# Optimization experiments

Measured on AMD Instinct MI355X. Metric: run time of the kernel, lower is better.

Reference implementation:

```python
import jax, jax.numpy as jnp
import numpy as np

KERNEL_SIZE = 32
STRIDE = 16


def _block_compress(x, w, pe):
    # x: [B, N, H, D]; w: [K]; pe: [K, D]
    B, N, H, D = x.shape
    M = (N - KERNEL_SIZE) // STRIDE + 1
    # window gather indices: [M, K]
    idx = jnp.arange(M)[:, None] * STRIDE + jnp.arange(KERNEL_SIZE)[None, :]
    xw = x[:, idx]  # [B, M, K, H, D]
    # y = sum_k w[k] * (x_window + pe) / kernel_size
    return jnp.einsum('bmkhd,k->bmhd', xw + pe[None, None, :, None, :], w) / KERNEL_SIZE


def setup_inputs() -> dict:
    key = jax.random.key(0)
    k1, k2, k3, k4, k5, k6, k7 = jax.random.split(key, 7)
    B, N, QH, KH, D, VD = 1, 8192, 32, 2, 128, 128
    return {
        'q': jax.random.normal(k1, (B, N, QH, D), dtype=jnp.float32),
        'k': jax.random.normal(k2, (B, N, KH, D), dtype=jnp.float32),
        'v': jax.random.normal(k3, (B, N, KH, VD), dtype=jnp.float32),
        'w_key': jax.random.normal(k4, (KERNEL_SIZE,), dtype=jnp.float32),
        'pe_key': jax.random.normal(k5, (KERNEL_SIZE, D), dtype=jnp.float32),
        'w_val': jax.random.normal(k6, (KERNEL_SIZE,), dtype=jnp.float32),
        'pe_val': jax.random.normal(k7, (KERNEL_SIZE, VD), dtype=jnp.float32),
    }


def reference(q, k, v, w_key, pe_key, w_val, pe_val):
    ck = _block_compress(k, w_key, pe_key)  # [B, M, KH, D]
    cv = _block_compress(v, w_val, pe_val)  # [B, M, KH, VD]
    B, N, QH, D = q.shape
    M, KH = ck.shape[1], ck.shape[2]
    G = QH // KH  # GQA group size; off_kh = off_qh // G -> qh index = kh*G + g
    sm_scale = D ** -0.5
    qg = q.reshape(B, N, KH, G, D)
    # scores: [B, KH, G, N, M]
    scores = jnp.einsum('bnhgd,bmhd->bhgnm', qg, ck) * sm_scale
    # block-causal mask: query n attends block m iff n >= m*stride + kernel_size - 1
    n_idx = jnp.arange(N)
    m_last = jnp.arange(M) * STRIDE + KERNEL_SIZE - 1
    mask = n_idx[:, None] >= m_last[None, :]  # [N, M]
    scores = jnp.where(mask[None, None, None], scores, -jnp.inf)
    lse = jax.nn.logsumexp(scores, axis=-1)  # [B, KH, G, N]
    # queries before kernel_size-1 have no valid blocks: kernel zeros o and lse
    valid = n_idx >= KERNEL_SIZE - 1
    lse = jnp.where(valid[None, None, None], lse, 0.0)
    p = jnp.exp(scores - lse[..., None])  # exp(-inf - 0) = 0 on invalid rows
    o = jnp.einsum('bhgnm,bmhd->bnhgd', p, cv).reshape(B, N, QH, -1)
    lse = lse.reshape(B, QH, N)
    return o, lse, ck
```

## Files before the change

kernel.cpp:

```cpp
#include <hip/hip_runtime.h>

#define DI __device__ __forceinline__

using f32x4  = __attribute__((ext_vector_type(4))) float;
using bf16x8 = __attribute__((ext_vector_type(8))) short;
using u32x4  = __attribute__((ext_vector_type(4))) unsigned int;

DI unsigned short f2bf(float f) {
    unsigned int u = __float_as_uint(f);
    unsigned int r = u + 0x7FFFu + ((u >> 16) & 1u);
    return (unsigned short)(r >> 16);
}

DI void gload_lds16(const void* g, void* l) {
    __builtin_amdgcn_global_load_lds(
        (const __attribute__((address_space(1))) void*)(unsigned long long)g,
        (__attribute__((address_space(3))) void*)(unsigned int)(unsigned long long)l,
        16, 0, 0);
}

constexpr int N_SEQ = 8192;
constexpr int QH    = 32;
constexpr int KH    = 2;
constexpr int D     = 128;
constexpr int M_CMP = 511;
constexpr int MP    = 512;
constexpr int NCH   = 16;
constexpr int CHUNK_ELEMS = 16 * 64 * 8;
constexpr int HSTRIDE = NCH * CHUNK_ELEMS;

__global__ __launch_bounds__(256)
void compress_kernel(const float* __restrict__ kin, const float* __restrict__ vin,
                     const float* __restrict__ w_key, const float* __restrict__ pe_key,
                     const float* __restrict__ w_val, const float* __restrict__ pe_val,
                     float* __restrict__ ck_out,
                     unsigned short* __restrict__ kvb)
{
    const int m  = blockIdx.x;
    const int t  = threadIdx.x;
    const int hh = t >> 7;
    const int d  = t & 127;
    float acck = 0.f, accv = 0.f;
    if (m < M_CMP) {
        #pragma unroll
        for (int k = 0; k < 32; ++k) {
            float xk = kin[((m*16 + k)*KH + hh)*D + d];
            float xv = vin[((m*16 + k)*KH + hh)*D + d];
            acck += (xk + pe_key[k*D + d]) * w_key[k];
            accv += (xv + pe_val[k*D + d]) * w_val[k];
        }
        acck *= (1.f/32.f);
        accv *= (1.f/32.f);
        ck_out[(m*KH + hh)*D + d] = acck;
    }
    const int c = m >> 5, ml = m & 31;
    {
        const int mt = ml >> 4, colx = ml & 15;
        const int kc = d >> 5, hix = (d >> 3) & 3, e = d & 7;
        kvb[(size_t)hh*HSTRIDE + (((c*16 + mt*4 + kc)*64) + hix*16 + colx)*8 + e] = f2bf(acck);
    }
    {
        const int e   = ((ml >> 4) << 2) + (ml & 3);
        const int hix = (ml >> 2) & 3;
        const int dt  = d >> 4, colx = d & 15;
        kvb[(size_t)hh*HSTRIDE + (((c*16 + 8 + dt)*64) + hix*16 + colx)*8 + e] = f2bf(accv);
    }
}

__global__ __launch_bounds__(256)
void attn_kernel(const float* __restrict__ q,
                 const unsigned short* __restrict__ kvb,
                 float* __restrict__ o,
                 float* __restrict__ lse)
{
    __shared__ __align__(16) unsigned short lds[2][16][64][8];

    const int h    = blockIdx.y;
    const int t    = threadIdx.x;
    const int wid  = t >> 6;
    const int lane = t & 63;
    const int col  = lane & 15;
    const int hi   = lane >> 4;
    const int j    = (blockIdx.x << 2) + wid;

    const int n0r = j;
    const int n1r = N_SEQ - 1 - j;
    const int mcnt0 = (n0r >= 31) ? (((n0r - 31) >> 4) + 1) : 0;
    const int mcnt1 = ((n1r - 31) >> 4) + 1;
    const int n1max = N_SEQ - 1 - (blockIdx.x << 2);
    const int nchb  = (((((n1max - 31) >> 4) + 1) + 31) >> 5);

    const float sm_scale = 0.08838834764831845f;
    const float NEG_INF  = -__builtin_inff();

    bf16x8 qf0[4], qf1[4];
    {
        const float* qp0 = q + ((size_t)n0r*QH + (h << 4) + col)*D + (hi << 3);
        const float* qp1 = q + ((size_t)n1r*QH + (h << 4) + col)*D + (hi << 3);
        #pragma unroll
        for (int kc = 0; kc < 4; ++kc) {
            float4 a0 = *(const float4*)(qp0 + kc*32);
            float4 b0 = *(const float4*)(qp0 + kc*32 + 4);
            float4 a1 = *(const float4*)(qp1 + kc*32);
            float4 b1 = *(const float4*)(qp1 + kc*32 + 4);
            bf16x8 f0, f1;
            f0[0]=(short)f2bf(a0.x*sm_scale); f0[1]=(short)f2bf(a0.y*sm_scale);
            f0[2]=(short)f2bf(a0.z*sm_scale); f0[3]=(short)f2bf(a0.w*sm_scale);
            f0[4]=(short)f2bf(b0.x*sm_scale); f0[5]=(short)f2bf(b0.y*sm_scale);
            f0[6]=(short)f2bf(b0.z*sm_scale); f0[7]=(short)f2bf(b0.w*sm_scale);
            f1[0]=(short)f2bf(a1.x*sm_scale); f1[1]=(short)f2bf(a1.y*sm_scale);
            f1[2]=(short)f2bf(a1.z*sm_scale); f1[3]=(short)f2bf(a1.w*sm_scale);
            f1[4]=(short)f2bf(b1.x*sm_scale); f1[5]=(short)f2bf(b1.y*sm_scale);
            f1[6]=(short)f2bf(b1.z*sm_scale); f1[7]=(short)f2bf(b1.w*sm_scale);
            qf0[kc] = f0; qf1[kc] = f1;
        }
    }

    f32x4 oacc0[8], oacc1[8];
    #pragma unroll
    for (int dt = 0; dt < 8; ++dt) {
        oacc0[dt] = (f32x4){0.f,0.f,0.f,0.f};
        oacc1[dt] = (f32x4){0.f,0.f,0.f,0.f};
    }
    float rmax0 = -3e38f, rmax1 = -3e38f, rsum0 = 0.f, rsum1 = 0.f;

    const unsigned short* kvh = kvb + (size_t)h*HSTRIDE;

    auto STAGE = [&](int buf, int c) {
        const unsigned short* gp = kvh + ((size_t)(c*16 + (wid << 2))*64 + lane)*8;
        #pragma unroll
        for (int p = 0; p < 4; ++p)
            gload_lds16(gp + p*512, &lds[buf][(wid << 2) + p][lane][0]);
    };

    auto SMAX = [&](f32x4 sa, f32x4 sb, int lim, float& rm, float& rs,
                    f32x4* oaccr, unsigned int* pw) {
        float sv[8];
        if (lim < 32) {
            const int mb = hi << 2;
            #pragma unroll
            for (int jj = 0; jj < 4; ++jj) {
                sv[jj]     = (mb + jj      < lim) ? sa[jj] : NEG_INF;
                sv[4 + jj] = (mb + jj + 16 < lim) ? sb[jj] : NEG_INF;
            }
        } else {
            #pragma unroll
            for (int jj = 0; jj < 4; ++jj) { sv[jj] = sa[jj]; sv[4 + jj] = sb[jj]; }
        }
        float pm = fmaxf(fmaxf(fmaxf(sv[0],sv[1]), fmaxf(sv[2],sv[3])),
                         fmaxf(fmaxf(sv[4],sv[5]), fmaxf(sv[6],sv[7])));
        if (!__all(pm <= rm + 8.0f)) {
            float tm = pm;
            tm = fmaxf(tm, __shfl_xor(tm, 16));
            tm = fmaxf(tm, __shfl_xor(tm, 32));
            float nm = fmaxf(rm, tm);
            float sc = __expf(rm - nm);
            rs *= sc;
            #pragma unroll
            for (int dt = 0; dt < 8; ++dt) {
                oaccr[dt][0] *= sc; oaccr[dt][1] *= sc;
                oaccr[dt][2] *= sc; oaccr[dt][3] *= sc;
            }
            rm = nm;
        }
        float p[8];
        #pragma unroll
        for (int i = 0; i < 8; ++i) p[i] = __expf(sv[i] - rm);
        rs += ((p[0]+p[1]) + (p[2]+p[3])) + ((p[4]+p[5]) + (p[6]+p[7]));
        asm("v_cvt_pk_bf16_f32 %0, %1, %2" : "=v"(pw[0]) : "v"(p[0]), "v"(p[1]));
        asm("v_cvt_pk_bf16_f32 %0, %1, %2" : "=v"(pw[1]) : "v"(p[2]), "v"(p[3]));
        asm("v_cvt_pk_bf16_f32 %0, %1, %2" : "=v"(pw[2]) : "v"(p[4]), "v"(p[5]));
        asm("v_cvt_pk_bf16_f32 %0, %1, %2" : "=v"(pw[3]) : "v"(p[6]), "v"(p[7]));
    };

    STAGE(0, 0);
    __syncthreads();

    for (int c = 0; c < nchb; ++c) {
        if (c + 1 < nchb) STAGE((c + 1) & 1, c + 1);

        const int m0 = c << 5;
        const bool a1 = (m0 < mcnt1);
        const bool a0 = (m0 < mcnt0);
        const unsigned short (*L)[64][8] = lds[c & 1];

        f32x4 s10 = (f32x4){0,0,0,0}, s11 = (f32x4){0,0,0,0};
        f32x4 s00 = (f32x4){0,0,0,0}, s01 = (f32x4){0,0,0,0};
        #pragma unroll
        for (int kc = 0; kc < 4; ++kc) {
            bf16x8 ca = *(const bf16x8*)&L[kc][lane][0];
            bf16x8 cb = *(const bf16x8*)&L[4 + kc][lane][0];
            s10 = __builtin_amdgcn_mfma_f32_16x16x32_bf16(ca, qf1[kc], s10, 0, 0, 0);
            s11 = __builtin_amdgcn_mfma_f32_16x16x32_bf16(cb, qf1[kc], s11, 0, 0, 0);
            if (a0) {
                s00 = __builtin_amdgcn_mfma_f32_16x16x32_bf16(ca, qf0[kc], s00, 0, 0, 0);
                s01 = __builtin_amdgcn_mfma_f32_16x16x32_bf16(cb, qf0[kc], s01, 0, 0, 0);
            }
        }
        unsigned int pw1[4], pw0[4];
        if (a1) SMAX(s10, s11, mcnt1 - m0, rmax1, rsum1, oacc1, pw1);
        if (a0) SMAX(s00, s01, mcnt0 - m0, rmax0, rsum0, oacc0, pw0);

        {
            u32x4 b1v = {pw1[0], pw1[1], pw1[2], pw1[3]};
            u32x4 b0v = {pw0[0], pw0[1], pw0[2], pw0[3]};
            #pragma unroll
            for (int dt = 0; dt < 8; ++dt) {
                bf16x8 cv = *(const bf16x8*)&L[8 + dt][lane][0];
                if (a1)
                    asm("v_mfma_f32_16x16x32_bf16 %0, %1, %2, %0"
                        : "+v"(oacc1[dt]) : "v"(cv), "v"(b1v));
                if (a0)
                    asm("v_mfma_f32_16x16x32_bf16 %0, %1, %2, %0"
                        : "+v"(oacc0[dt]) : "v"(cv), "v"(b0v));
            }
        }

        __syncthreads();
    }

    auto EPI = [&](int n, float rm, float rs, f32x4* oaccr, bool valid) {
        float r = rs;
        r += __shfl_xor(r, 16);
        r += __shfl_xor(r, 32);
        const float inv = valid ? (1.0f / r) : 0.0f;
        float* op = o + ((size_t)n*QH + (h << 4) + col)*D + (hi << 2);
        #pragma unroll
        for (int dt = 0; dt < 8; ++dt) {
            f32x4 w = oaccr[dt];
            w[0] *= inv; w[1] *= inv; w[2] *= inv; w[3] *= inv;
            *(f32x4*)(op + dt*16) = w;
        }
        if (lane < 16) {
            float lv = valid ? (rm + __logf(r)) : 0.0f;
            lse[((size_t)(h << 4) + col)*N_SEQ + n] = lv;
        }
    };
    EPI(n0r, rmax0, rsum0, oacc0, mcnt0 > 0);
    EPI(n1r, rmax1, rsum1, oacc1, true);
}

extern "C" void kernel_launch(void* const* d_in, const int* in_sizes, int n_in,
                              void* d_out, int out_size, void* d_ws, size_t ws_size,
                              hipStream_t stream)
{
    const float* q      = (const float*)d_in[0];
    const float* k      = (const float*)d_in[1];
    const float* v      = (const float*)d_in[2];
    const float* w_key  = (const float*)d_in[3];
    const float* pe_key = (const float*)d_in[4];
    const float* w_val  = (const float*)d_in[5];
    const float* pe_val = (const float*)d_in[6];

    float* o   = (float*)d_out;
    float* lse = o + (size_t)N_SEQ * QH * D;
    float* ck  = lse + (size_t)QH * N_SEQ;

    unsigned short* kvb = (unsigned short*)d_ws;

    compress_kernel<<<dim3(MP), dim3(256), 0, stream>>>(
        k, v, w_key, pe_key, w_val, pe_val, ck, kvb);

    attn_kernel<<<dim3(N_SEQ/8, KH), dim3(256), 0, stream>>>(
        q, kvb, o, lse);
}
```

Baseline: 100.5 us.

## Split KV chunks across two wave groups and merge softmax states via LDS

The block grows to 512 threads with two 4-wave groups. Each group processes alternating KV chunks, so the per-query KV loop is split in two. The groups then merge partial max, sum and output accumulators through shared memory before the epilogue. This aims to shorten the serial chunk loop and raise the number of waves in flight, at the cost of larger LDS use (68KB), lower block occupancy and an extra merge phase with barriers.

```diff
diff --git a/kernel.cpp b/kernel.cpp
--- a/kernel.cpp
+++ b/kernel.cpp
@@ -67,21 +67,23 @@
     }
 }
 
-__global__ __launch_bounds__(256)
+__global__ __launch_bounds__(512)
 void attn_kernel(const float* __restrict__ q,
                  const unsigned short* __restrict__ kvb,
                  float* __restrict__ o,
                  float* __restrict__ lse)
 {
-    __shared__ __align__(16) unsigned short lds[2][16][64][8];
+    __shared__ __align__(16) unsigned char smem[69632];
 
     const int h    = blockIdx.y;
     const int t    = threadIdx.x;
     const int wid  = t >> 6;
+    const int grp  = wid >> 2;
+    const int lw   = wid & 3;
     const int lane = t & 63;
     const int col  = lane & 15;
     const int hi   = lane >> 4;
-    const int j    = (blockIdx.x << 2) + wid;
+    const int j    = (blockIdx.x << 2) + lw;
 
     const int n0r = j;
     const int n1r = N_SEQ - 1 - j;
@@ -89,9 +91,14 @@
     const int mcnt1 = ((n1r - 31) >> 4) + 1;
     const int n1max = N_SEQ - 1 - (blockIdx.x << 2);
     const int nchb  = (((((n1max - 31) >> 4) + 1) + 31) >> 5);
+    const int T     = (nchb + 1) >> 1;
 
     const float sm_scale = 0.08838834764831845f;
     const float NEG_INF  = -__builtin_inff();
+
+    auto SB = [&](int idx) {
+        return (unsigned short (*)[64][8])(smem + idx * 16384);
+    };
 
     bf16x8 qf0[4], qf1[4];
     {
@@ -126,11 +133,12 @@
 
     const unsigned short* kvh = kvb + (size_t)h*HSTRIDE;
 
-    auto STAGE = [&](int buf, int c) {
-        const unsigned short* gp = kvh + ((size_t)(c*16 + (wid << 2))*64 + lane)*8;
+    auto STAGE = [&](int bufidx, int c) {
+        const unsigned short* gp = kvh + ((size_t)(c*16 + (lw << 2))*64 + lane)*8;
+        unsigned short (*L)[64][8] = SB(bufidx);
         #pragma unroll
         for (int p = 0; p < 4; ++p)
-            gload_lds16(gp + p*512, &lds[buf][(wid << 2) + p][lane][0]);
+            gload_lds16(gp + p*512, &L[(lw << 2) + p][lane][0]);
     };
 
     auto SMAX = [&](f32x4 sa, f32x4 sb, int lim, float& rm, float& rs,
@@ -173,35 +181,42 @@
         asm("v_cvt_pk_bf16_f32 %0, %1, %2" : "=v"(pw[3]) : "v"(p[6]), "v"(p[7]));
     };
 
-    STAGE(0, 0);
-    __syncthreads();
-
-    for (int c = 0; c < nchb; ++c) {
-        if (c + 1 < nchb) STAGE((c + 1) & 1, c + 1);
-
-        const int m0 = c << 5;
-        const bool a1 = (m0 < mcnt1);
-        const bool a0 = (m0 < mcnt0);
-        const unsigned short (*L)[64][8] = lds[c & 1];
-
-        f32x4 s10 = (f32x4){0,0,0,0}, s11 = (f32x4){0,0,0,0};
-        f32x4 s00 = (f32x4){0,0,0,0}, s01 = (f32x4){0,0,0,0};
-        #pragma unroll
-        for (int kc = 0; kc < 4; ++kc) {
-            bf16x8 ca = *(const bf16x8*)&L[kc][lane][0];
-            bf16x8 cb = *(const bf16x8*)&L[4 + kc][lane][0];
-            s10 = __builtin_amdgcn_mfma_f32_16x16x32_bf16(ca, qf1[kc], s10, 0, 0, 0);
-            s11 = __builtin_amdgcn_mfma_f32_16x16x32_bf16(cb, qf1[kc], s11, 0, 0, 0);
-            if (a0) {
-                s00 = __builtin_amdgcn_mfma_f32_16x16x32_bf16(ca, qf0[kc], s00, 0, 0, 0);
-                s01 = __builtin_amdgcn_mfma_f32_16x16x32_bf16(cb, qf0[kc], s01, 0, 0, 0);
-            }
-        }
-        unsigned int pw1[4], pw0[4];
-        if (a1) SMAX(s10, s11, mcnt1 - m0, rmax1, rsum1, oacc1, pw1);
-        if (a0) SMAX(s00, s01, mcnt0 - m0, rmax0, rsum0, oacc0, pw0);
-
-        {
+    STAGE(grp*2 + 0, grp);
+
+    for (int tt = 0; tt < T; ++tt) {
+        const int c = 2*tt + grp;
+        const bool live = (c < nchb);
+
+        asm volatile("s_waitcnt vmcnt(0)" ::: "memory");
+        __builtin_amdgcn_s_barrier();
+        __builtin_amdgcn_sched_barrier(0);
+
+        int cs = c + 2; if (cs > nchb - 1) cs = nchb - 1;
+        STAGE(grp*2 + ((tt + 1) & 1), cs);
+
+        if (live) {
+            const int m0 = c << 5;
+            const bool a1 = (m0 < mcnt1);
+            const bool a0 = (m0 < mcnt0);
+            const unsigned short (*L)[64][8] = SB(grp*2 + (tt & 1));
+
+            f32x4 s10 = (f32x4){0,0,0,0}, s11 = (f32x4){0,0,0,0};
+            f32x4 s00 = (f32x4){0,0,0,0}, s01 = (f32x4){0,0,0,0};
+            #pragma unroll
+            for (int kc = 0; kc < 4; ++kc) {
+                bf16x8 ca = *(const bf16x8*)&L[kc][lane][0];
+                bf16x8 cb = *(const bf16x8*)&L[4 + kc][lane][0];
+                s10 = __builtin_amdgcn_mfma_f32_16x16x32_bf16(ca, qf1[kc], s10, 0, 0, 0);
+                s11 = __builtin_amdgcn_mfma_f32_16x16x32_bf16(cb, qf1[kc], s11, 0, 0, 0);
+                if (a0) {
+                    s00 = __builtin_amdgcn_mfma_f32_16x16x32_bf16(ca, qf0[kc], s00, 0, 0, 0);
+                    s01 = __builtin_amdgcn_mfma_f32_16x16x32_bf16(cb, qf0[kc], s01, 0, 0, 0);
+                }
+            }
+            unsigned int pw1[4], pw0[4];
+            if (a1) SMAX(s10, s11, mcnt1 - m0, rmax1, rsum1, oacc1, pw1);
+            if (a0) SMAX(s00, s01, mcnt0 - m0, rmax0, rsum0, oacc0, pw0);
+
             u32x4 b1v = {pw1[0], pw1[1], pw1[2], pw1[3]};
             u32x4 b0v = {pw0[0], pw0[1], pw0[2], pw0[3]};
             #pragma unroll
@@ -215,29 +230,73 @@
                         : "+v"(oacc0[dt]) : "v"(cv), "v"(b0v));
             }
         }
-
-        __syncthreads();
-    }
-
-    auto EPI = [&](int n, float rm, float rs, f32x4* oaccr, bool valid) {
-        float r = rs;
-        r += __shfl_xor(r, 16);
-        r += __shfl_xor(r, 32);
-        const float inv = valid ? (1.0f / r) : 0.0f;
-        float* op = o + ((size_t)n*QH + (h << 4) + col)*D + (hi << 2);
-        #pragma unroll
-        for (int dt = 0; dt < 8; ++dt) {
-            f32x4 w = oaccr[dt];
-            w[0] *= inv; w[1] *= inv; w[2] *= inv; w[3] *= inv;
-            *(f32x4*)(op + dt*16) = w;
-        }
-        if (lane < 16) {
-            float lv = valid ? (rm + __logf(r)) : 0.0f;
-            lse[((size_t)(h << 4) + col)*N_SEQ + n] = lv;
-        }
-    };
-    EPI(n0r, rmax0, rsum0, oacc0, mcnt0 > 0);
-    EPI(n1r, rmax1, rsum1, oacc1, true);
+    }
+
+    __syncthreads();
+    float* oM  = (float*)smem;
+    float* mlM = (float*)(smem + 65536);
+    if (grp == 1) {
+        const int base = ((lw << 6) + lane) << 6;
+        #pragma unroll
+        for (int dt = 0; dt < 8; ++dt)
+            #pragma unroll
+            for (int jj = 0; jj < 4; ++jj) {
+                oM[base + dt*4 + jj]      = oacc0[dt][jj];
+                oM[base + 32 + dt*4 + jj] = oacc1[dt][jj];
+            }
+        const int mb = ((lw << 6) + lane) << 2;
+        mlM[mb + 0] = rmax0; mlM[mb + 1] = rsum0;
+        mlM[mb + 2] = rmax1; mlM[mb + 3] = rsum1;
+    }
+    __syncthreads();
+    if (grp == 0) {
+        const int base = ((lw << 6) + lane) << 6;
+        const int mb   = ((lw << 6) + lane) << 2;
+        {
+            float m1 = mlM[mb + 0], l1 = mlM[mb + 1];
+            float m  = fmaxf(rmax0, m1);
+            float s0 = __expf(rmax0 - m), s1 = __expf(m1 - m);
+            rsum0 = rsum0 * s0 + l1 * s1;
+            rmax0 = m;
+            #pragma unroll
+            for (int dt = 0; dt < 8; ++dt)
+                #pragma unroll
+                for (int jj = 0; jj < 4; ++jj)
+                    oacc0[dt][jj] = oacc0[dt][jj]*s0 + oM[base + dt*4 + jj]*s1;
+        }
+        {
+            float m1 = mlM[mb + 2], l1 = mlM[mb + 3];
+            float m  = fmaxf(rmax1, m1);
+            float s0 = __expf(rmax1 - m), s1 = __expf(m1 - m);
+            rsum1 = rsum1 * s0 + l1 * s1;
+            rmax1 = m;
+            #pragma unroll
+            for (int dt = 0; dt < 8; ++dt)
+                #pragma unroll
+                for (int jj = 0; jj < 4; ++jj)
+                    oacc1[dt][jj] = oacc1[dt][jj]*s0 + oM[base + 32 + dt*4 + jj]*s1;
+        }
+
+        auto EPI = [&](int n, float rm, float rs, f32x4* oaccr, bool valid) {
+            float r = rs;
+            r += __shfl_xor(r, 16);
+            r += __shfl_xor(r, 32);
+            const float inv = valid ? (1.0f / r) : 0.0f;
+            float* op = o + ((size_t)n*QH + (h << 4) + col)*D + (hi << 2);
+            #pragma unroll
+            for (int dt = 0; dt < 8; ++dt) {
+                f32x4 w = oaccr[dt];
+                w[0] *= inv; w[1] *= inv; w[2] *= inv; w[3] *= inv;
+                *(f32x4*)(op + dt*16) = w;
+            }
+            if (lane < 16) {
+                float lv = valid ? (rm + __logf(r)) : 0.0f;
+                lse[((size_t)(h << 4) + col)*N_SEQ + n] = lv;
+            }
+        };
+        EPI(n0r, rmax0, rsum0, oacc0, mcnt0 > 0);
+        EPI(n1r, rmax1, rsum1, oacc1, true);
+    }
 }
 
 extern "C" void kernel_launch(void* const* d_in, const int* in_sizes, int n_in,
@@ -261,6 +320,6 @@
     compress_kernel<<<dim3(MP), dim3(256), 0, stream>>>(
         k, v, w_key, pe_key, w_val, pe_val, ck, kvb);
 
-    attn_kernel<<<dim3(N_SEQ/8, KH), dim3(256), 0, stream>>>(
+    attn_kernel<<<dim3(N_SEQ/8, KH), dim3(512), 0, stream>>>(
         q, kvb, o, lse);
 }
```

Result: slower. 160.7 us (+59.9%).
